# Performance work log

Measured on AMD Instinct MI355X. Metric: run time of the kernel, lower is better.

The kernel has to match this reference:

```python
import jax, jax.numpy as jnp
import numpy as np

DIM = 1024
HEADS = 16
HEAD_DIM = DIM // HEADS
D_FF = 4 * DIM
EPS = 1e-5


def _layernorm(x, g, b):
    mu = jnp.mean(x, axis=-1, keepdims=True)
    var = jnp.mean(jnp.square(x - mu), axis=-1, keepdims=True)
    return (x - mu) * jax.lax.rsqrt(var + EPS) * g + b


def setup_inputs() -> dict:
    key = jax.random.key(0)
    ks = jax.random.split(key, 8)
    s = 0.02
    return {
        "x": jax.random.normal(ks[0], (2, 2048, DIM), dtype=jnp.float32),
        "Wqkv": jax.random.normal(ks[1], (DIM, 3 * DIM), dtype=jnp.float32) * s,
        "bqkv": jnp.zeros((3 * DIM,), dtype=jnp.float32),
        "Wout": jax.random.normal(ks[2], (DIM, DIM), dtype=jnp.float32) * s,
        "bout": jnp.zeros((DIM,), dtype=jnp.float32),
        "W1": jax.random.normal(ks[3], (DIM, D_FF), dtype=jnp.float32) * s,
        "b1": jnp.zeros((D_FF,), dtype=jnp.float32),
        "W2": jax.random.normal(ks[4], (D_FF, DIM), dtype=jnp.float32) * s,
        "b2": jnp.zeros((DIM,), dtype=jnp.float32),
        "g1": jnp.ones((DIM,), dtype=jnp.float32),
        "be1": jnp.zeros((DIM,), dtype=jnp.float32),
        "g2": jnp.ones((DIM,), dtype=jnp.float32),
        "be2": jnp.zeros((DIM,), dtype=jnp.float32),
    }


def reference(x, Wqkv, bqkv, Wout, bout, W1, b1, W2, b2, g1, be1, g2, be2):
    B, T, C = x.shape
    # --- multi-head self-attention (explicit QK^T softmax, no mask/cache) ---
    qkv = (x @ Wqkv + bqkv).reshape(B, T, 3, HEADS, HEAD_DIM)
    q = qkv[:, :, 0].transpose(0, 2, 1, 3)  # (B,H,T,hd)
    k = qkv[:, :, 1].transpose(0, 2, 1, 3)
    v = qkv[:, :, 2].transpose(0, 2, 1, 3)
    scale = HEAD_DIM ** -0.5
    scores = jnp.einsum("bhqd,bhkd->bhqk", q, k) * scale  # (B,H,T,T)
    attn = jax.nn.softmax(scores, axis=-1)
    o = jnp.einsum("bhqk,bhkd->bhqd", attn, v)
    o = o.transpose(0, 2, 1, 3).reshape(B, T, C)
    attn_out = o @ Wout + bout
    # --- Post-LN: LN applied to sublayer output, then residual ---
    x = x + _layernorm(attn_out, g1, be1)
    # --- FFN with exact GELU ---
    h = jax.nn.gelu(x @ W1 + b1, approximate=False)
    ffn_out = h @ W2 + b2
    x = x + _layernorm(ffn_out, g2, be2)
    return x
```

## Files before the change

kernel.cpp:

```cpp
#include <hip/hip_runtime.h>
#include <cstdint>
#include <cstddef>

#define DIM 1024
#define HEADS 16
#define HD 64
#define DFF 4096
#define TSEQ 2048
#define EPS 1e-5f

#define WAITCNT_VM4 0xF74
#define WAITCNT_VM0 0xF70
#define WAITCNT_VM8 0xF78
#define WAITCNT_LGKM0 0xC07F

typedef __bf16 bf16x8 __attribute__((ext_vector_type(8)));
typedef float floatx4 __attribute__((ext_vector_type(4)));

__device__ __forceinline__ unsigned short f2bf(float f) {
  union { float f; unsigned int u; } v; v.f = f;
  return (unsigned short)((v.u + 0x7FFFu + ((v.u >> 16) & 1u)) >> 16);
}

__device__ __forceinline__ float exp2_fast(float x) {
#if __has_builtin(__builtin_amdgcn_exp2f)
  return __builtin_amdgcn_exp2f(x);
#else
  float r;
  asm("v_exp_f32 %0, %1" : "=v"(r) : "v"(x));
  return r;
#endif
}

__device__ __forceinline__ float gelu_f(float v) {
  const float u = v * (0.7978845608f + 0.0356774081f * v * v);
  const float e = __expf(2.0f * u);
  const float t = 1.0f - 2.0f / (e + 1.0f);
  return 0.5f * v * (1.0f + t);
}

__device__ __forceinline__ void async16(const void* g, void* l) {
  __builtin_amdgcn_global_load_lds(
      (const __attribute__((address_space(1))) void*)g,
      (__attribute__((address_space(3))) void*)l, 16, 0, 0);
}

__global__ __launch_bounds__(256) void prep_all(const float* __restrict__ x,
                                                const float* __restrict__ Wqkv,
                                                const float* __restrict__ Wout,
                                                const float* __restrict__ W1,
                                                const float* __restrict__ W2,
                                                unsigned short* __restrict__ xb,
                                                unsigned short* __restrict__ WqkvT,
                                                unsigned short* __restrict__ WoutT,
                                                unsigned short* __restrict__ W1T,
                                                unsigned short* __restrict__ W2T) {
  const int bid = blockIdx.x;
  const int tid = threadIdx.x;
  if (bid < 4096) {
    const int i = bid * 256 + tid;
    float4 v = ((const float4*)x)[i];
    ushort4 o;
    o.x = f2bf(v.x); o.y = f2bf(v.y); o.z = f2bf(v.z); o.w = f2bf(v.w);
    ((ushort4*)xb)[i] = o;
    return;
  }
  int id = bid - 4096;
  const float* src; unsigned short* dst; int R, C, gx;
  if (id < 3072)      {            src = Wqkv; dst = WqkvT; R = 1024; C = 3072; gx = 96; }
  else if (id < 4096) { id -= 3072; src = Wout; dst = WoutT; R = 1024; C = 1024; gx = 32; }
  else if (id < 8192) { id -= 4096; src = W1;   dst = W1T;   R = 1024; C = 4096; gx = 128; }
  else                { id -= 8192; src = W2;   dst = W2T;   R = 4096; C = 1024; gx = 32; }
  const int c0 = (id % gx) * 32, r0 = (id / gx) * 32;
  const int tx = tid & 31, ty = tid >> 5;
  __shared__ float tile[32][33];
#pragma unroll
  for (int i = 0; i < 32; i += 8)
    tile[ty + i][tx] = src[(size_t)(r0 + ty + i) * C + c0 + tx];
  __syncthreads();
#pragma unroll
  for (int i = 0; i < 32; i += 8)
    dst[(size_t)(c0 + ty + i) * R + r0 + tx] = f2bf(tile[tx][ty + i]);
}

#define PIPELINED_KLOOP3(NIT)                                                        \
  auto issue = [&](int s, int k0) {                                                  \
    async16(Ab0 + k0, &lds[s][tid * 8]);                                             \
    async16(Ab1 + k0, &lds[s][2048 + tid * 8]);                                      \
    async16(Bb0 + k0, &lds[s][4096 + tid * 8]);                                      \
    async16(Bb1 + k0, &lds[s][6144 + tid * 8]);                                      \
  };                                                                                 \
  issue(0, 0);                                                                       \
  issue(1, 32);                                                                      \
  int sidx = 0;                                                                      \
  for (int k = 0; k < (NIT); k++) {                                                  \
    if (k < (NIT)-1) __builtin_amdgcn_s_waitcnt(WAITCNT_VM4);                        \
    else             __builtin_amdgcn_s_waitcnt(WAITCNT_VM0);                        \
    __builtin_amdgcn_s_barrier();                                                    \
    if (k + 2 < (NIT)) {                                                             \
      int s2 = sidx + 2; if (s2 >= 3) s2 -= 3;                                       \
      issue(s2, (k + 2) * 32);                                                       \
    }                                                                                \
    bf16x8 af[4], bg[4];                                                             \
    _Pragma("unroll")                                                                \
    for (int mi = 0; mi < 4; mi++)                                                   \
      af[mi] = *(const bf16x8*)&lds[sidx][(wm + mi * 16 + l16) * 32 + quad * 8];     \
    _Pragma("unroll")                                                                \
    for (int ni = 0; ni < 4; ni++)                                                   \
      bg[ni] = *(const bf16x8*)&lds[sidx][4096 + (wn + ni * 16 + l16) * 32 + quad * 8]; \
    _Pragma("unroll")                                                                \
    for (int mi = 0; mi < 4; mi++)                                                   \
      _Pragma("unroll")                                                              \
      for (int ni = 0; ni < 4; ni++)                                                 \
        acc[mi][ni] =                                                                \
            __builtin_amdgcn_mfma_f32_16x16x32_bf16(af[mi], bg[ni], acc[mi][ni], 0, 0, 0); \
    sidx = (sidx == 2) ? 0 : sidx + 1;                                               \
  }

#define PIPELINED_KLOOP2(NIT)                                                        \
  auto issue = [&](int s, int k0) {                                                  \
    async16(Ab0 + k0, &lds[s][tid * 8]);                                             \
    async16(Ab1 + k0, &lds[s][2048 + tid * 8]);                                      \
    async16(Bb0 + k0, &lds[s][4096 + tid * 8]);                                      \
    async16(Bb1 + k0, &lds[s][6144 + tid * 8]);                                      \
  };                                                                                 \
  issue(0, 0);                                                                       \
  int sidx = 0;                                                                      \
  for (int k = 0; k < (NIT); k++) {                                                  \
    if (k + 1 < (NIT)) {                                                             \
      issue(sidx ^ 1, (k + 1) * 32);                                                 \
      __builtin_amdgcn_s_waitcnt(WAITCNT_VM4);                                       \
    } else {                                                                         \
      __builtin_amdgcn_s_waitcnt(WAITCNT_VM0);                                       \
    }                                                                                \
    __builtin_amdgcn_s_barrier();                                                    \
    bf16x8 af[4], bg[4];                                                             \
    _Pragma("unroll")                                                                \
    for (int mi = 0; mi < 4; mi++)                                                   \
      af[mi] = *(const bf16x8*)&lds[sidx][(wm + mi * 16 + l16) * 32 + quad * 8];     \
    _Pragma("unroll")                                                                \
    for (int ni = 0; ni < 4; ni++)                                                   \
      bg[ni] = *(const bf16x8*)&lds[sidx][4096 + (wn + ni * 16 + l16) * 32 + quad * 8]; \
    _Pragma("unroll")                                                                \
    for (int mi = 0; mi < 4; mi++)                                                   \
      _Pragma("unroll")                                                              \
      for (int ni = 0; ni < 4; ni++)                                                 \
        acc[mi][ni] =                                                                \
            __builtin_amdgcn_mfma_f32_16x16x32_bf16(af[mi], bg[ni], acc[mi][ni], 0, 0, 0); \
    __builtin_amdgcn_s_waitcnt(WAITCNT_LGKM0);                                       \
    __builtin_amdgcn_s_barrier();                                                    \
    sidx ^= 1;                                                                       \
  }

template <int EPI>
__global__ __launch_bounds__(256) void gemm_bt(const unsigned short* __restrict__ A,
                                               const unsigned short* __restrict__ Bt,
                                               const float* __restrict__ bias,
                                               void* __restrict__ Cout,
                                               int M, int N, int K) {
  __shared__ unsigned short lds[2][8192];
  const int tid = threadIdx.x;
  const int bm = blockIdx.y * 128, bn = blockIdx.x * 128;
  const int wave = tid >> 6, lane = tid & 63;
  const int l16 = lane & 15, quad = lane >> 4;
  const int wm = (wave >> 1) * 64, wn = (wave & 1) * 64;

  floatx4 acc[4][4] = {};

  const int srow = tid >> 2;
  const int scol = (tid & 3) * 8;

  const unsigned short* Ab0 = A + (size_t)(bm + srow) * K + scol;
  const unsigned short* Ab1 = A + (size_t)(bm + 64 + srow) * K + scol;
  const unsigned short* Bb0 = Bt + (size_t)(bn + srow) * K + scol;
  const unsigned short* Bb1 = Bt + (size_t)(bn + 64 + srow) * K + scol;

  const int nit = K >> 5;
  PIPELINED_KLOOP2(nit)
  __syncthreads();

  if (EPI == 0) {
#pragma unroll
    for (int ni = 0; ni < 4; ni++) {
      const int col = bn + wn + ni * 16 + l16;
      const float bv = bias[col];
#pragma unroll
      for (int mi = 0; mi < 4; mi++) {
        const int row0 = bm + wm + mi * 16 + quad * 4;
#pragma unroll
        for (int r = 0; r < 4; r++)
          ((float*)Cout)[(size_t)(row0 + r) * N + col] = acc[mi][ni][r] + bv;
      }
    }
  } else {
    unsigned short* eb = &lds[0][wave * 1152];
    float bvv[4];
#pragma unroll
    for (int ni = 0; ni < 4; ni++) bvv[ni] = bias[bn + wn + ni * 16 + l16];
    const int lrow = lane >> 2, ck = lane & 3;
#pragma unroll
    for (int mi = 0; mi < 4; mi++) {
#pragma unroll
      for (int ni = 0; ni < 4; ni++)
#pragma unroll
        for (int r = 0; r < 4; r++)
          eb[(quad * 4 + r) * 72 + ni * 16 + l16] =
              f2bf(gelu_f(acc[mi][ni][r] + bvv[ni]));
      __syncthreads();
      unsigned short* gp =
          (unsigned short*)Cout + (size_t)(bm + wm + mi * 16 + lrow) * N + bn + wn;
#pragma unroll
      for (int j = 0; j < 2; j++)
        *(uint4*)(gp + j * 32 + ck * 8) = *(const uint4*)&eb[lrow * 72 + j * 32 + ck * 8];
      __syncthreads();
    }
  }
}

__global__ __launch_bounds__(256) void gemm_splitk(const unsigned short* __restrict__ A,
                                                   const unsigned short* __restrict__ Bt,
                                                   float* __restrict__ Cp,
                                                   int M, int N, int Ktot, int Ksl) {
  __shared__ unsigned short lds[3][8192];
  const int tid = threadIdx.x;
  const int bm = blockIdx.y * 128, bn = blockIdx.x * 128;
  const int koff = blockIdx.z * Ksl;
  const int wave = tid >> 6, lane = tid & 63;
  const int l16 = lane & 15, quad = lane >> 4;
  const int wm = (wave >> 1) * 64, wn = (wave & 1) * 64;

  floatx4 acc[4][4] = {};

  const int srow = tid >> 2;
  const int scol = (tid & 3) * 8;

  const unsigned short* Ab0 = A + (size_t)(bm + srow) * Ktot + koff + scol;
  const unsigned short* Ab1 = A + (size_t)(bm + 64 + srow) * Ktot + koff + scol;
  const unsigned short* Bb0 = Bt + (size_t)(bn + srow) * Ktot + koff + scol;
  const unsigned short* Bb1 = Bt + (size_t)(bn + 64 + srow) * Ktot + koff + scol;

  const int nit = Ksl >> 5;
  PIPELINED_KLOOP3(nit)

  float* out = Cp + (size_t)blockIdx.z * M * (size_t)N;
#pragma unroll
  for (int ni = 0; ni < 4; ni++) {
    const int col = bn + wn + ni * 16 + l16;
#pragma unroll
    for (int mi = 0; mi < 4; mi++) {
      const int row0 = bm + wm + mi * 16 + quad * 4;
#pragma unroll
      for (int r = 0; r < 4; r++)
        out[(size_t)(row0 + r) * N + col] = acc[mi][ni][r];
    }
  }
}

__global__ __launch_bounds__(256) void gemm_qkv(const unsigned short* __restrict__ A,
                                                const unsigned short* __restrict__ Bt,
                                                const float* __restrict__ bias,
                                                unsigned short* __restrict__ Qg,
                                                unsigned short* __restrict__ Kg,
                                                unsigned short* __restrict__ Vtg) {
  const int K = 1024;
  __shared__ unsigned short lds[3][8192];
  const int tid = threadIdx.x;
  const int bm = blockIdx.y * 128, bn = blockIdx.x * 128;
  const int wave = tid >> 6, lane = tid & 63;
  const int l16 = lane & 15, quad = lane >> 4;
  const int wm = (wave >> 1) * 64, wn = (wave & 1) * 64;

  floatx4 acc[4][4] = {};

  const int srow = tid >> 2;
  const int scol = (tid & 3) * 8;

  const unsigned short* Ab0 = A + (size_t)(bm + srow) * K + scol;
  const unsigned short* Ab1 = A + (size_t)(bm + 64 + srow) * K + scol;
  const unsigned short* Bb0 = Bt + (size_t)(bn + srow) * K + scol;
  const unsigned short* Bb1 = Bt + (size_t)(bn + 64 + srow) * K + scol;

  const int nit = K >> 5;
  PIPELINED_KLOOP3(nit)

  const float QSCALE = 0.125f * 1.44269504089f;
#pragma unroll
  for (int ni = 0; ni < 4; ni++) {
    const int col = bn + wn + ni * 16 + l16;
    const float bv = bias[col];
    const int sec = col >> 10;
    const int cc = col & 1023;
    const int hh = cc >> 6, dd = cc & 63;
#pragma unroll
    for (int mi = 0; mi < 4; mi++) {
      const int row0 = bm + wm + mi * 16 + quad * 4;
      const int b2 = row0 >> 11, tt0 = row0 & 2047;
      if (sec == 0) {
        unsigned short* q = Qg + ((size_t)(b2 * HEADS + hh) * TSEQ + tt0) * HD + dd;
#pragma unroll
        for (int r = 0; r < 4; r++)
          q[(size_t)r * HD] = f2bf((acc[mi][ni][r] + bv) * QSCALE);
      } else if (sec == 1) {
        unsigned short* k = Kg + ((size_t)(b2 * HEADS + hh) * TSEQ + tt0) * HD + dd;
#pragma unroll
        for (int r = 0; r < 4; r++)
          k[(size_t)r * HD] = f2bf(acc[mi][ni][r] + bv);
      } else {
        ushort4 o;
        o.x = f2bf(acc[mi][ni][0] + bv);
        o.y = f2bf(acc[mi][ni][1] + bv);
        o.z = f2bf(acc[mi][ni][2] + bv);
        o.w = f2bf(acc[mi][ni][3] + bv);
        *(ushort4*)(Vtg + ((size_t)(b2 * HEADS + hh) * HD + dd) * TSEQ + tt0) = o;
      }
    }
  }
}

__global__ __launch_bounds__(256, 4) void attn_mfma(const unsigned short* __restrict__ Qg,
                                                    const unsigned short* __restrict__ Kg,
                                                    const unsigned short* __restrict__ Vtg,
                                                    unsigned short* __restrict__ ob) {
  __shared__ __align__(16) char smem[40960];
  unsigned short* QPs = (unsigned short*)smem;

  const int bid = blockIdx.x;
  const int lid = (bid & 7) * 128 + (bid >> 3);
  const int qt = lid & 31;
  const int h = (lid >> 5) & 15;
  const int b = lid >> 9;
  const int tid = threadIdx.x;
  const int w = tid >> 6, lane = tid & 63, l16 = lane & 15, quad = lane >> 4;
  const int qg = w >> 1;
  const int kh = w & 1;

  const int r0 = tid >> 3;
  const int c0 = (tid & 7) ^ (r0 & 7);

  const char* Qbase = (const char*)(Qg + ((size_t)(b * HEADS + h) * TSEQ + qt * 64) * HD);
  const char* Kbase = (const char*)(Kg + (size_t)(b * HEADS + h) * TSEQ * HD);
  const char* Vbase = (const char*)(Vtg + (size_t)(b * HEADS + h) * HD * TSEQ);

  auto Ksp = [&](int s) -> char* { return smem + 8192 + s * 8192; };
  auto Vsp = [&](int s) -> char* { return smem + 24576 + s * 8192; };

  auto issueKV = [&](int s, int ch) {
    const size_t koff = (size_t)ch * 64;
#pragma unroll
    for (int i = 0; i < 2; i++) {
      async16(Kbase + (koff + r0 + i * 32) * 128 + c0 * 16, Ksp(s) + (i * 256 + tid) * 16);
      async16(Vbase + (size_t)(r0 + i * 32) * (TSEQ * 2) + koff * 2 + c0 * 16,
              Vsp(s) + (i * 256 + tid) * 16);
    }
  };

#pragma unroll
  for (int i = 0; i < 2; i++)
    async16(Qbase + (size_t)(r0 + i * 32) * 128 + c0 * 16, (char*)QPs + (i * 256 + tid) * 16);
  issueKV(0, 0);
  issueKV(1, 1);

  __builtin_amdgcn_s_waitcnt(WAITCNT_VM8);
  __builtin_amdgcn_s_barrier();

  bf16x8 qf[2][2];
#pragma unroll
  for (int mi = 0; mi < 2; mi++)
#pragma unroll
    for (int kt = 0; kt < 2; kt++) {
      const int row = qg * 32 + mi * 16 + l16;
      qf[mi][kt] = *(const bf16x8*)((const char*)QPs + row * 128 +
                                    (((quad + 4 * kt) ^ (row & 7)) * 16));
    }
  __builtin_amdgcn_s_waitcnt(WAITCNT_LGKM0);
  __builtin_amdgcn_sched_barrier(0);

  union { unsigned short u[8]; bf16x8 b; } onesu;
#pragma unroll
  for (int j = 0; j < 8; j++) onesu.u[j] = 0x3F80;
  const bf16x8 ones = onesu.b;

  floatx4 oacc[2][5] = {};
  char* Pw = (char*)QPs + w * 2048;

  const int NC = TSEQ / 64;
  int sidx = 0;
  for (int ch = 0; ch < NC; ch++) {
    if (ch < NC - 1) __builtin_amdgcn_s_waitcnt(WAITCNT_VM4);
    else             __builtin_amdgcn_s_waitcnt(WAITCNT_VM0);
    __builtin_amdgcn_s_barrier();

    floatx4 sacc[2][2] = {};
    __builtin_amdgcn_s_setprio(1);
#pragma unroll
    for (int kt = 0; kt < 2; kt++) {
#pragma unroll
      for (int ni = 0; ni < 2; ni++) {
        const int krow = kh * 32 + ni * 16 + l16;
        bf16x8 kf = *(const bf16x8*)(Ksp(sidx) + krow * 128 +
                                     (((quad + 4 * kt) ^ (krow & 7)) * 16));
#pragma unroll
        for (int mi = 0; mi < 2; mi++)
          sacc[mi][ni] =
              __builtin_amdgcn_mfma_f32_16x16x32_bf16(qf[mi][kt], kf, sacc[mi][ni], 0, 0, 0);
      }
    }
    __builtin_amdgcn_s_setprio(0);

#pragma unroll
    for (int mi = 0; mi < 2; mi++)
#pragma unroll
      for (int ni = 0; ni < 2; ni++)
#pragma unroll
        for (int r = 0; r < 4; r++) {
          const float p = exp2_fast(sacc[mi][ni][r]);
          const unsigned int pu = __builtin_bit_cast(unsigned int, p);
          const int row = mi * 16 + quad * 4 + r;
          *((unsigned short*)(Pw + row * 64 +
                              (((ni * 2 + (l16 >> 3)) ^ quad) * 16) + (l16 & 7) * 2)) =
              (unsigned short)(pu >> 16);
        }

    __builtin_amdgcn_s_setprio(1);
    bf16x8 pf[2];
#pragma unroll
    for (int mi = 0; mi < 2; mi++) {
      const int prow = mi * 16 + l16;
      pf[mi] = *(const bf16x8*)(Pw + prow * 64 + ((quad ^ ((l16 >> 2) & 3)) * 16));
    }
#pragma unroll
    for (int nj = 0; nj < 4; nj++) {
      const int vrow = nj * 16 + l16;
      bf16x8 vf = *(const bf16x8*)(Vsp(sidx) + vrow * 128 +
                                   (((quad + 4 * kh) ^ (vrow & 7)) * 16));
#pragma unroll
      for (int mi = 0; mi < 2; mi++)
        oacc[mi][nj] = __builtin_amdgcn_mfma_f32_16x16x32_bf16(pf[mi], vf, oacc[mi][nj], 0, 0, 0);
    }
#pragma unroll
    for (int mi = 0; mi < 2; mi++)
      oacc[mi][4] = __builtin_amdgcn_mfma_f32_16x16x32_bf16(pf[mi], ones, oacc[mi][4], 0, 0, 0);
    __builtin_amdgcn_s_setprio(0);

    __builtin_amdgcn_s_waitcnt(WAITCNT_LGKM0);
    __builtin_amdgcn_s_barrier();
    if (ch + 2 < NC) issueKV(sidx, ch + 2);
    sidx ^= 1;
  }

  __syncthreads();
  float* Op = (float*)smem + qg * (32 * 66);
  if (kh == 1) {
#pragma unroll
    for (int mi = 0; mi < 2; mi++)
#pragma unroll
      for (int r = 0; r < 4; r++) {
        const int row = mi * 16 + quad * 4 + r;
#pragma unroll
        for (int nj = 0; nj < 4; nj++)
          Op[row * 66 + nj * 16 + l16] = oacc[mi][nj][r];
        if (l16 == 0) Op[row * 66 + 64] = oacc[mi][4][r];
      }
  }
  __syncthreads();
  if (kh == 0) {
#pragma unroll
    for (int mi = 0; mi < 2; mi++)
#pragma unroll
      for (int r = 0; r < 4; r++) {
        const int row = mi * 16 + quad * 4 + r;
        const float inv = 1.0f / (oacc[mi][4][r] + Op[row * 66 + 64]);
        const int t = qt * 64 + qg * 32 + row;
        unsigned short* orow = ob + (size_t)(b * TSEQ + t) * DIM + h * HD + l16;
#pragma unroll
        for (int nj = 0; nj < 4; nj++)
          orow[nj * 16] = f2bf((oacc[mi][nj][r] + Op[row * 66 + nj * 16 + l16]) * inv);
      }
  }
}

template <int NP, int WBF>
__global__ __launch_bounds__(256) void add_ln_red(const float* __restrict__ xin,
                                                  const float* __restrict__ parts,
                                                  const float* __restrict__ bias,
                                                  const float* __restrict__ gw,
                                                  const float* __restrict__ bw,
                                                  float* __restrict__ xout,
                                                  unsigned short* __restrict__ xbf) {
  const size_t MN = (size_t)4096 * DIM;
  const int row = blockIdx.x;
  const int tid = threadIdx.x;
  const int c = tid * 4;
  const size_t base = (size_t)row * DIM;
  float4 v = *(const float4*)(parts + base + c);
#pragma unroll
  for (int p = 1; p < NP; p++) {
    float4 t = *(const float4*)(parts + p * MN + base + c);
    v.x += t.x; v.y += t.y; v.z += t.z; v.w += t.w;
  }
  float4 bb = *(const float4*)(bias + c);
  v.x += bb.x; v.y += bb.y; v.z += bb.z; v.w += bb.w;

  float s = v.x + v.y + v.z + v.w;
  float s2 = v.x * v.x + v.y * v.y + v.z * v.z + v.w * v.w;
#pragma unroll
  for (int off = 1; off < 64; off <<= 1) {
    s += __shfl_xor(s, off);
    s2 += __shfl_xor(s2, off);
  }
  __shared__ float rsum[4], rsq[4];
  if ((tid & 63) == 0) { rsum[tid >> 6] = s; rsq[tid >> 6] = s2; }
  __syncthreads();
  s = rsum[0] + rsum[1] + rsum[2] + rsum[3];
  s2 = rsq[0] + rsq[1] + rsq[2] + rsq[3];
  const float mu = s * (1.0f / DIM);
  const float var = s2 * (1.0f / DIM) - mu * mu;
  const float rstd = rsqrtf(var + EPS);
  float4 xv = *(const float4*)(xin + base + c);
  float4 gv = *(const float4*)(gw + c);
  float4 bv = *(const float4*)(bw + c);
  float4 o;
  o.x = xv.x + (v.x - mu) * rstd * gv.x + bv.x;
  o.y = xv.y + (v.y - mu) * rstd * gv.y + bv.y;
  o.z = xv.z + (v.z - mu) * rstd * gv.z + bv.z;
  o.w = xv.w + (v.w - mu) * rstd * gv.w + bv.w;
  *(float4*)(xout + base + c) = o;
  if (WBF) {
    ushort4 ob;
    ob.x = f2bf(o.x); ob.y = f2bf(o.y); ob.z = f2bf(o.z); ob.w = f2bf(o.w);
    *(ushort4*)(xbf + base + c) = ob;
  }
}

extern "C" void kernel_launch(void* const* d_in, const int* in_sizes, int n_in,
                              void* d_out, int out_size, void* d_ws, size_t ws_size,
                              hipStream_t stream) {
  const float* x    = (const float*)d_in[0];
  const float* Wqkv = (const float*)d_in[1];
  const float* bqkv = (const float*)d_in[2];
  const float* Wout = (const float*)d_in[3];
  const float* bout = (const float*)d_in[4];
  const float* W1   = (const float*)d_in[5];
  const float* b1   = (const float*)d_in[6];
  const float* W2   = (const float*)d_in[7];
  const float* b2   = (const float*)d_in[8];
  const float* g1   = (const float*)d_in[9];
  const float* be1  = (const float*)d_in[10];
  const float* g2   = (const float*)d_in[11];
  const float* be2  = (const float*)d_in[12];

  char* w = (char*)d_ws;
  const size_t MB = 1048576;
  unsigned short* xb     = (unsigned short*)(w + 0 * MB);
  unsigned short* WqkvT  = (unsigned short*)(w + 8 * MB);
  unsigned short* WoutT  = (unsigned short*)(w + 14 * MB);
  unsigned short* W1T    = (unsigned short*)(w + 16 * MB);
  unsigned short* W2T    = (unsigned short*)(w + 24 * MB);
  unsigned short* Qb     = (unsigned short*)(w + 32 * MB);
  unsigned short* Kb     = (unsigned short*)(w + 40 * MB);
  unsigned short* Vtb    = (unsigned short*)(w + 48 * MB);
  unsigned short* obuf   = (unsigned short*)(w + 64 * MB);
  float*          atno_p = (float*)(w + 72 * MB);
  float*          x1     = (float*)(w + 104 * MB);
  unsigned short* x1b    = (unsigned short*)(w + 120 * MB);
  unsigned short* hb     = (unsigned short*)(w + 128 * MB);
  float*          ffn_p  = (float*)(w + 32 * MB);

  prep_all<<<16384, 256, 0, stream>>>(x, Wqkv, Wout, W1, W2, xb, WqkvT, WoutT, W1T, W2T);

  gemm_qkv<<<dim3(24, 32), 256, 0, stream>>>(xb, WqkvT, bqkv, Qb, Kb, Vtb);
  attn_mfma<<<1024, 256, 0, stream>>>(Qb, Kb, Vtb, obuf);
  gemm_splitk<<<dim3(8, 32, 2), 256, 0, stream>>>(obuf, WoutT, atno_p, 4096, 1024, 1024, 512);
  add_ln_red<2, 1><<<4096, 256, 0, stream>>>(x, atno_p, bout, g1, be1, x1, x1b);
  gemm_bt<1><<<dim3(32, 32), 256, 0, stream>>>(x1b, W1T, b1, hb, 4096, 4096, 1024);
  gemm_splitk<<<dim3(8, 32, 2), 256, 0, stream>>>(hb, W2T, ffn_p, 4096, 1024, 4096, 2048);
  add_ln_red<2, 0><<<4096, 256, 0, stream>>>(x1, ffn_p, b2, g2, be2, (float*)d_out, nullptr);
}
```

Measured before the change: 363.0 us.

## Remap GEMM blocks per XCD for L2 locality and shrink attention P scratch

Three GEMM kernels (gemm_bt, gemm_splitk, gemm_qkv) now remap block indices so that blocks dispatched round-robin to the same XCD cover a compact 2D tile region. Neighbouring tiles then share A/B panels in that XCD's L2. Separately, the attention P-tile staging in LDS now uses a 16-row padded buffer (stride 72 bytes) reused per mi instead of a 32-row swizzled one, which lowers LDS footprint per wave. The remapping hardcodes grid shapes, and the reused per-mi buffer adds a write-then-read dependency within each wave without a barrier.

```diff
diff --git a/kernel.cpp b/kernel.cpp
--- a/kernel.cpp
+++ b/kernel.cpp
@@ -15,6 +15,7 @@
 #define WAITCNT_LGKM0 0xC07F
 
 typedef __bf16 bf16x8 __attribute__((ext_vector_type(8)));
+typedef __bf16 bf16x4 __attribute__((ext_vector_type(4)));
 typedef float floatx4 __attribute__((ext_vector_type(4)));
 
 __device__ __forceinline__ unsigned short f2bf(float f) {
@@ -160,7 +161,14 @@
                                                int M, int N, int K) {
   __shared__ unsigned short lds[2][8192];
   const int tid = threadIdx.x;
-  const int bm = blockIdx.y * 128, bn = blockIdx.x * 128;
+  int bxx = blockIdx.x, byy = blockIdx.y;
+  if (gridDim.x == 32 && gridDim.y == 32) {
+    const int id = byy * 32 + bxx;
+    const int xcd = id & 7, sub = id >> 3;
+    bxx = (xcd & 3) * 8 + (sub & 7);
+    byy = (xcd >> 2) * 16 + (sub >> 3);
+  }
+  const int bm = byy * 128, bn = bxx * 128;
   const int wave = tid >> 6, lane = tid & 63;
   const int l16 = lane & 15, quad = lane >> 4;
   const int wm = (wave >> 1) * 64, wn = (wave & 1) * 64;
@@ -223,8 +231,13 @@
                                                    int M, int N, int Ktot, int Ksl) {
   __shared__ unsigned short lds[3][8192];
   const int tid = threadIdx.x;
-  const int bm = blockIdx.y * 128, bn = blockIdx.x * 128;
-  const int koff = blockIdx.z * Ksl;
+  const int id = (blockIdx.z * 32 + blockIdx.y) * 8 + blockIdx.x;
+  const int xcd = id & 7, sub = id >> 3;
+  const int bxx = sub & 7;
+  const int byz = xcd * (gridDim.z * 4) + (sub >> 3);
+  const int byy = byz & 31, bz = byz >> 5;
+  const int bm = byy * 128, bn = bxx * 128;
+  const int koff = bz * Ksl;
   const int wave = tid >> 6, lane = tid & 63;
   const int l16 = lane & 15, quad = lane >> 4;
   const int wm = (wave >> 1) * 64, wn = (wave & 1) * 64;
@@ -242,7 +255,7 @@
   const int nit = Ksl >> 5;
   PIPELINED_KLOOP3(nit)
 
-  float* out = Cp + (size_t)blockIdx.z * M * (size_t)N;
+  float* out = Cp + (size_t)bz * M * (size_t)N;
 #pragma unroll
   for (int ni = 0; ni < 4; ni++) {
     const int col = bn + wn + ni * 16 + l16;
@@ -265,7 +278,11 @@
   const int K = 1024;
   __shared__ unsigned short lds[3][8192];
   const int tid = threadIdx.x;
-  const int bm = blockIdx.y * 128, bn = blockIdx.x * 128;
+  const int id = blockIdx.y * 24 + blockIdx.x;
+  const int xcd = id & 7, sub = id >> 3;
+  const int bxx = (xcd & 3) * 6 + sub % 6;
+  const int byy = (xcd >> 2) * 16 + sub / 6;
+  const int bm = byy * 128, bn = bxx * 128;
   const int wave = tid >> 6, lane = tid & 63;
   const int l16 = lane & 15, quad = lane >> 4;
   const int wm = (wave >> 1) * 64, wn = (wave & 1) * 64;
@@ -381,7 +398,7 @@
   const bf16x8 ones = onesu.b;
 
   floatx4 oacc[2][5] = {};
-  char* Pw = (char*)QPs + w * 2048;
+  char* Pw = (char*)QPs + w * 1152;
 
   const int NC = TSEQ / 64;
   int sidx = 0;
@@ -407,27 +424,25 @@
     }
     __builtin_amdgcn_s_setprio(0);
 
-#pragma unroll
-    for (int mi = 0; mi < 2; mi++)
+    bf16x8 pf[2];
+#pragma unroll
+    for (int mi = 0; mi < 2; mi++) {
 #pragma unroll
       for (int ni = 0; ni < 2; ni++)
 #pragma unroll
         for (int r = 0; r < 4; r++) {
           const float p = exp2_fast(sacc[mi][ni][r]);
           const unsigned int pu = __builtin_bit_cast(unsigned int, p);
-          const int row = mi * 16 + quad * 4 + r;
-          *((unsigned short*)(Pw + row * 64 +
-                              (((ni * 2 + (l16 >> 3)) ^ quad) * 16) + (l16 & 7) * 2)) =
+          *((unsigned short*)(Pw + (quad * 4 + r) * 72 + (ni * 16 + l16) * 2)) =
               (unsigned short)(pu >> 16);
         }
+      union { bf16x8 v8; bf16x4 v4[2]; } u;
+      u.v4[0] = *(const bf16x4*)(Pw + l16 * 72 + quad * 16);
+      u.v4[1] = *(const bf16x4*)(Pw + l16 * 72 + quad * 16 + 8);
+      pf[mi] = u.v8;
+    }
 
     __builtin_amdgcn_s_setprio(1);
-    bf16x8 pf[2];
-#pragma unroll
-    for (int mi = 0; mi < 2; mi++) {
-      const int prow = mi * 16 + l16;
-      pf[mi] = *(const bf16x8*)(Pw + prow * 64 + ((quad ^ ((l16 >> 2) & 3)) * 16));
-    }
 #pragma unroll
     for (int nj = 0; nj < 4; nj++) {
       const int vrow = nj * 16 + l16;
```

Measured after the change: 341.3 us (median of 3 runs). -6.0%, faster.
